# Optimization experiments

Measured on AMD Instinct MI355X. Metric: run time of the kernel, lower is better.

Reference implementation:

```python
import jax, jax.numpy as jnp
import numpy as np


def setup_inputs() -> dict:
    key = jax.random.key(0)
    k_x, k_w1, k_w2 = jax.random.split(key, 3)
    b, d, m, h = 256, 2048, 64, 128  # batch, d_model, history_length, d_out
    lim1 = 1.0 / np.sqrt(m + h)
    lim2 = 1.0 / np.sqrt(h + d)
    x = jax.random.normal(k_x, (b, d, m), dtype=jnp.float32)
    w1 = jax.random.uniform(k_w1, (m, h, d), dtype=jnp.float32, minval=-lim1, maxval=lim1)
    b1 = jnp.zeros((1, h, d), dtype=jnp.float32)
    w2 = jax.random.uniform(k_w2, (h, d), dtype=jnp.float32, minval=-lim2, maxval=lim2)
    b2 = jnp.zeros((1, h), dtype=jnp.float32)
    return {"x": x, "w1": w1, "b1": b1, "w2": w2, "b2": b2}


def reference(x, w1, b1, w2, b2):
    # per-neuron (per-d) MLP: contract over history m, then over hidden h
    hidden = jnp.einsum('bdm,mhd->bhd', x, w1) + b1  # (b, h, d)
    out = jnp.einsum('bhd,hd->bh', hidden, w2) + b2  # (b, h)
    return out
```

## Files before the change

kernel.cpp:

```cpp
#include <hip/hip_runtime.h>

typedef unsigned short u16;
typedef __attribute__((ext_vector_type(8))) short short8;
typedef __attribute__((ext_vector_type(4))) float f32x4;

#define D_TOT 2048
#define M_TOT 64
#define H_TOT 128
#define B_TOT 256
#define NG    256
#define XB    131072
#define W1M   262144

__device__ __forceinline__ u16 f2bf(float f) {
  unsigned u = __builtin_bit_cast(unsigned, f);
  u = (u + 0x7fffu + ((u >> 16) & 1u)) >> 16;
  return (u16)u;
}
__device__ __forceinline__ float bf2f(u16 v) {
  unsigned u = ((unsigned)v) << 16;
  return __builtin_bit_cast(float, u);
}

__global__ __launch_bounds__(256)
void nlm_p0(const float* __restrict__ b1, const float* __restrict__ w2,
            const float* __restrict__ b2, float* __restrict__ ch) {
  const int h = blockIdx.x, t = threadIdx.x;
  const float4* pb = (const float4*)(b1 + (size_t)h * D_TOT);
  const float4* pw = (const float4*)(w2 + (size_t)h * D_TOT);
  float s = 0.f;
  for (int i = t; i < D_TOT / 4; i += 256) {
    float4 a = pb[i], w = pw[i];
    s += a.x * w.x + a.y * w.y + a.z * w.z + a.w * w.w;
  }
  __shared__ float red[256];
  red[t] = s;
  __syncthreads();
  for (int off = 128; off > 0; off >>= 1) {
    if (t < off) red[t] += red[t + off];
    __syncthreads();
  }
  if (t == 0) ch[h] = red[0] + b2[h];
}

__global__ __launch_bounds__(512, 2)
void nlm_main(const float* __restrict__ x, const float* __restrict__ w1,
              const float* __restrict__ w2, u16* __restrict__ partial) {
  __shared__ __align__(16) u16 Bs[8 * H_TOT * 64];
  __shared__ __align__(16) u16 As[2][64 * 72];

  const int tid  = threadIdx.x;
  const int lane = tid & 63, wave = tid >> 6;
  const int g    = ((blockIdx.x & 7) << 5) + (blockIdx.x >> 3);
  const int d0   = g * 8;

  const int a_bl = tid >> 3, a_p = tid & 7;
  const float* xbase = x + (size_t)a_bl * XB + (size_t)d0 * M_TOT + a_p * 8;

  float4 e0 = *(const float4*)(xbase);
  float4 e1 = *(const float4*)(xbase + 4);

  {
    const int m = lane;
#pragma unroll 4
    for (int rep = 0; rep < 16; ++rep) {
      const int h = wave * 16 + rep;
      const float* w1p = w1 + (size_t)m * W1M + (size_t)h * D_TOT + d0;
      const float* w2p = w2 + (size_t)h * D_TOT + d0;
      float4 a0 = *(const float4*)(w1p);
      float4 a1 = *(const float4*)(w1p + 4);
      float4 s0 = *(const float4*)(w2p);
      float4 s1 = *(const float4*)(w2p + 4);
      u16* dst = (u16*)((char*)Bs + h * 128 + ((m * 2) ^ ((h & 7) << 4)));
      dst[0 * 8192] = f2bf(a0.x * s0.x);
      dst[1 * 8192] = f2bf(a0.y * s0.y);
      dst[2 * 8192] = f2bf(a0.z * s0.z);
      dst[3 * 8192] = f2bf(a0.w * s0.w);
      dst[4 * 8192] = f2bf(a1.x * s1.x);
      dst[5 * 8192] = f2bf(a1.y * s1.y);
      dst[6 * 8192] = f2bf(a1.z * s1.z);
      dst[7 * 8192] = f2bf(a1.w * s1.w);
    }
  }
  __syncthreads();

  const int wm = wave >> 2, wn = wave & 3;
  const int quad = lane >> 4, l16 = lane & 15;
  const int q16 = quad * 16;

  int aoff[2][2];
#pragma unroll
  for (int i = 0; i < 2; ++i)
#pragma unroll
    for (int s = 0; s < 2; ++s)
      aoff[i][s] = (wm * 32 + i * 16 + l16) * 72 + s * 32 + quad * 8;

  int boff[2][2];
#pragma unroll
  for (int j = 0; j < 2; ++j) {
    const int hr = wn * 32 + j * 16 + l16;
    const int bx = (hr & 7) << 4;
#pragma unroll
    for (int s = 0; s < 2; ++s)
      boff[j][s] = hr * 128 + ((s * 64 + q16) ^ bx);
  }

  {
    short8 av;
    av[0] = (short)f2bf(e0.x); av[1] = (short)f2bf(e0.y);
    av[2] = (short)f2bf(e0.z); av[3] = (short)f2bf(e0.w);
    av[4] = (short)f2bf(e1.x); av[5] = (short)f2bf(e1.y);
    av[6] = (short)f2bf(e1.z); av[7] = (short)f2bf(e1.w);
    *(short8*)(&As[0][0] + a_bl * 72 + a_p * 8) = av;
  }
  float4 p00, p01, p10, p11;
  {
    const float* xp = xbase + 1 * M_TOT;
    p10 = *(const float4*)(xp);
    p11 = *(const float4*)(xp + 4);
  }
  asm volatile("s_waitcnt lgkmcnt(0)" ::: "memory");
  __builtin_amdgcn_s_barrier();

  f32x4 acc[2][2];

  for (int bq = 0; bq < 4; ++bq) {
#pragma unroll
    for (int i = 0; i < 2; ++i)
#pragma unroll
      for (int j = 0; j < 2; ++j) acc[i][j] = (f32x4){0.f, 0.f, 0.f, 0.f};

#pragma unroll
    for (int c = 0; c < 8; ++c) {
      if (bq < 3 || c < 6) {
        const int bq2 = (c < 6) ? bq : bq + 1;
        const int c2  = (c < 6) ? c + 2 : c - 6;
        const float* xp = xbase + (size_t)bq2 * (64 * (size_t)XB) + c2 * M_TOT;
        if ((c & 1) == 0) { p00 = *(const float4*)(xp); p01 = *(const float4*)(xp + 4); }
        else              { p10 = *(const float4*)(xp); p11 = *(const float4*)(xp + 4); }
      }
      {
        const u16*  Ab = &As[c & 1][0];
        const char* Bb = (const char*)Bs + c * 16384;
#pragma unroll
        for (int s = 0; s < 2; ++s) {
          short8 af0 = *(const short8*)(Ab + aoff[0][s]);
          short8 af1 = *(const short8*)(Ab + aoff[1][s]);
          short8 bf0 = *(const short8*)(Bb + boff[0][s]);
          short8 bf1 = *(const short8*)(Bb + boff[1][s]);
          acc[0][0] = __builtin_amdgcn_mfma_f32_16x16x32_bf16(af0, bf0, acc[0][0], 0, 0, 0);
          acc[0][1] = __builtin_amdgcn_mfma_f32_16x16x32_bf16(af0, bf1, acc[0][1], 0, 0, 0);
          acc[1][0] = __builtin_amdgcn_mfma_f32_16x16x32_bf16(af1, bf0, acc[1][0], 0, 0, 0);
          acc[1][1] = __builtin_amdgcn_mfma_f32_16x16x32_bf16(af1, bf1, acc[1][1], 0, 0, 0);
        }
      }
      if (bq < 3 || c < 7) {
        float4 s0 = ((c + 1) & 1) ? p10 : p00;
        float4 s1 = ((c + 1) & 1) ? p11 : p01;
        short8 av;
        av[0] = (short)f2bf(s0.x); av[1] = (short)f2bf(s0.y);
        av[2] = (short)f2bf(s0.z); av[3] = (short)f2bf(s0.w);
        av[4] = (short)f2bf(s1.x); av[5] = (short)f2bf(s1.y);
        av[6] = (short)f2bf(s1.z); av[7] = (short)f2bf(s1.w);
        *(short8*)(&As[(c + 1) & 1][0] + a_bl * 72 + a_p * 8) = av;
      }
      asm volatile("s_waitcnt lgkmcnt(0)" ::: "memory");
      __builtin_amdgcn_s_barrier();
    }

#pragma unroll
    for (int i = 0; i < 2; ++i)
#pragma unroll
      for (int j = 0; j < 2; ++j) {
        const int hcol = wn * 32 + j * 16 + l16;
#pragma unroll
        for (int r = 0; r < 4; ++r) {
          const int brow = bq * 64 + wm * 32 + i * 16 + quad * 4 + r;
          partial[((size_t)brow * NG + g) * H_TOT + hcol] = f2bf(acc[i][j][r]);
        }
      }
  }
}

__global__ __launch_bounds__(256)
void nlm_p2(const u16* __restrict__ partial, const float* __restrict__ ch,
            float* __restrict__ out) {
  const int b = blockIdx.x, t = threadIdx.x;
  const int h2   = t & 63;
  const int half = t >> 6;
  const u16* base = partial + ((size_t)b * NG + half * 64) * H_TOT + 2 * h2;
  float s0 = 0.f, s1 = 0.f;
#pragma unroll 8
  for (int gg = 0; gg < 64; ++gg) {
    unsigned v = __builtin_nontemporal_load((const unsigned*)(base + (size_t)gg * H_TOT));
    s0 += bf2f((u16)(v & 0xffffu));
    s1 += bf2f((u16)(v >> 16));
  }
  __shared__ float red0[256], red1[256];
  red0[t] = s0;
  red1[t] = s1;
  __syncthreads();
  if (t < 64) {
    float a0 = red0[t] + red0[t + 64] + red0[t + 128] + red0[t + 192];
    float a1 = red1[t] + red1[t + 64] + red1[t + 128] + red1[t + 192];
    out[(size_t)b * H_TOT + 2 * t]     = a0 + ch[2 * t];
    out[(size_t)b * H_TOT + 2 * t + 1] = a1 + ch[2 * t + 1];
  }
}

extern "C" void kernel_launch(void* const* d_in, const int* in_sizes, int n_in,
                              void* d_out, int out_size, void* d_ws, size_t ws_size,
                              hipStream_t stream) {
  const float* x  = (const float*)d_in[0];
  const float* w1 = (const float*)d_in[1];
  const float* b1 = (const float*)d_in[2];
  const float* w2 = (const float*)d_in[3];
  const float* b2 = (const float*)d_in[4];
  float* out = (float*)d_out;

  u16*   partial = (u16*)d_ws;
  float* ch      = (float*)((char*)d_ws + (size_t)B_TOT * NG * H_TOT * sizeof(u16));

  nlm_p0<<<dim3(128),   dim3(256), 0, stream>>>(b1, w2, b2, ch);
  nlm_main<<<dim3(256), dim3(512), 0, stream>>>(x, w1, w2, partial);
  nlm_p2<<<dim3(256),   dim3(256), 0, stream>>>(partial, ch, out);
}
```

Baseline: 266.3 us.

## Load x fragments directly into registers, drop LDS A staging and barriers

The main kernel no longer stages x tiles through a double-buffered LDS array with per-step barriers. Each wave now owns 32 batch rows and all 128 hidden columns, loading its A fragments straight from global memory into registers and issuing 32 MFMAs per k-step. The per-wave tiling changes from 32x32 to 32x128, which raises accumulator register use and drops the software prefetch pipeline. That may expose global load latency and lower occupancy.

```diff
diff --git a/kernel.cpp b/kernel.cpp
--- a/kernel.cpp
+++ b/kernel.cpp
@@ -20,6 +20,14 @@
 __device__ __forceinline__ float bf2f(u16 v) {
   unsigned u = ((unsigned)v) << 16;
   return __builtin_bit_cast(float, u);
+}
+__device__ __forceinline__ short8 pack8(float4 a, float4 b) {
+  short8 t;
+  t[0] = (short)f2bf(a.x); t[1] = (short)f2bf(a.y);
+  t[2] = (short)f2bf(a.z); t[3] = (short)f2bf(a.w);
+  t[4] = (short)f2bf(b.x); t[5] = (short)f2bf(b.y);
+  t[6] = (short)f2bf(b.z); t[7] = (short)f2bf(b.w);
+  return t;
 }
 
 __global__ __launch_bounds__(256)
@@ -47,18 +55,25 @@
 void nlm_main(const float* __restrict__ x, const float* __restrict__ w1,
               const float* __restrict__ w2, u16* __restrict__ partial) {
   __shared__ __align__(16) u16 Bs[8 * H_TOT * 64];
-  __shared__ __align__(16) u16 As[2][64 * 72];
 
   const int tid  = threadIdx.x;
   const int lane = tid & 63, wave = tid >> 6;
   const int g    = ((blockIdx.x & 7) << 5) + (blockIdx.x >> 3);
   const int d0   = g * 8;
-
-  const int a_bl = tid >> 3, a_p = tid & 7;
-  const float* xbase = x + (size_t)a_bl * XB + (size_t)d0 * M_TOT + a_p * 8;
-
-  float4 e0 = *(const float4*)(xbase);
-  float4 e1 = *(const float4*)(xbase + 4);
+  const int quad = lane >> 4, l16 = lane & 15;
+
+  const int wb = wave * 32;
+  const float* xr0 = x + (size_t)(wb + l16) * XB + (size_t)d0 * M_TOT + quad * 8;
+  const float* xr1 = xr0 + (size_t)16 * XB;
+
+  float4 e00a = *(const float4*)(xr0);
+  float4 e00b = *(const float4*)(xr0 + 4);
+  float4 e01a = *(const float4*)(xr0 + 32);
+  float4 e01b = *(const float4*)(xr0 + 36);
+  float4 e10a = *(const float4*)(xr1);
+  float4 e10b = *(const float4*)(xr1 + 4);
+  float4 e11a = *(const float4*)(xr1 + 32);
+  float4 e11b = *(const float4*)(xr1 + 36);
 
   {
     const int m = lane;
@@ -82,104 +97,63 @@
       dst[7 * 8192] = f2bf(a1.w * s1.w);
     }
   }
+
+  int boff[8][2];
+#pragma unroll
+  for (int j = 0; j < 8; ++j) {
+    const int hr = j * 16 + l16;
+    const int bx = (hr & 7) << 4;
+    boff[j][0] = hr * 128 + ((quad * 16) ^ bx);
+    boff[j][1] = hr * 128 + ((64 + quad * 16) ^ bx);
+  }
+
+  f32x4 acc[2][8];
+#pragma unroll
+  for (int i = 0; i < 2; ++i)
+#pragma unroll
+    for (int j = 0; j < 8; ++j) acc[i][j] = (f32x4){0.f, 0.f, 0.f, 0.f};
+
   __syncthreads();
 
-  const int wm = wave >> 2, wn = wave & 3;
-  const int quad = lane >> 4, l16 = lane & 15;
-  const int q16 = quad * 16;
-
-  int aoff[2][2];
+#pragma unroll
+  for (int c = 0; c < 8; ++c) {
+    short8 a00, a01, a10, a11;
+    if (c == 0) {
+      a00 = pack8(e00a, e00b); a01 = pack8(e01a, e01b);
+      a10 = pack8(e10a, e10b); a11 = pack8(e11a, e11b);
+    } else {
+      const float* p0 = xr0 + c * M_TOT;
+      const float* p1 = xr1 + c * M_TOT;
+      a00 = pack8(*(const float4*)(p0),      *(const float4*)(p0 + 4));
+      a01 = pack8(*(const float4*)(p0 + 32), *(const float4*)(p0 + 36));
+      a10 = pack8(*(const float4*)(p1),      *(const float4*)(p1 + 4));
+      a11 = pack8(*(const float4*)(p1 + 32), *(const float4*)(p1 + 36));
+    }
+    const char* Bb = (const char*)Bs + c * 16384;
+#pragma unroll
+    for (int s = 0; s < 2; ++s) {
+      const short8 f0 = s ? a01 : a00;
+      const short8 f1 = s ? a11 : a10;
+#pragma unroll
+      for (int j = 0; j < 8; ++j) {
+        short8 bf = *(const short8*)(Bb + boff[j][s]);
+        acc[0][j] = __builtin_amdgcn_mfma_f32_16x16x32_bf16(f0, bf, acc[0][j], 0, 0, 0);
+        acc[1][j] = __builtin_amdgcn_mfma_f32_16x16x32_bf16(f1, bf, acc[1][j], 0, 0, 0);
+      }
+    }
+  }
+
 #pragma unroll
   for (int i = 0; i < 2; ++i)
 #pragma unroll
-    for (int s = 0; s < 2; ++s)
-      aoff[i][s] = (wm * 32 + i * 16 + l16) * 72 + s * 32 + quad * 8;
-
-  int boff[2][2];
-#pragma unroll
-  for (int j = 0; j < 2; ++j) {
-    const int hr = wn * 32 + j * 16 + l16;
-    const int bx = (hr & 7) << 4;
-#pragma unroll
-    for (int s = 0; s < 2; ++s)
-      boff[j][s] = hr * 128 + ((s * 64 + q16) ^ bx);
-  }
-
-  {
-    short8 av;
-    av[0] = (short)f2bf(e0.x); av[1] = (short)f2bf(e0.y);
-    av[2] = (short)f2bf(e0.z); av[3] = (short)f2bf(e0.w);
-    av[4] = (short)f2bf(e1.x); av[5] = (short)f2bf(e1.y);
-    av[6] = (short)f2bf(e1.z); av[7] = (short)f2bf(e1.w);
-    *(short8*)(&As[0][0] + a_bl * 72 + a_p * 8) = av;
-  }
-  float4 p00, p01, p10, p11;
-  {
-    const float* xp = xbase + 1 * M_TOT;
-    p10 = *(const float4*)(xp);
-    p11 = *(const float4*)(xp + 4);
-  }
-  asm volatile("s_waitcnt lgkmcnt(0)" ::: "memory");
-  __builtin_amdgcn_s_barrier();
-
-  f32x4 acc[2][2];
-
-  for (int bq = 0; bq < 4; ++bq) {
-#pragma unroll
-    for (int i = 0; i < 2; ++i)
-#pragma unroll
-      for (int j = 0; j < 2; ++j) acc[i][j] = (f32x4){0.f, 0.f, 0.f, 0.f};
-
-#pragma unroll
-    for (int c = 0; c < 8; ++c) {
-      if (bq < 3 || c < 6) {
-        const int bq2 = (c < 6) ? bq : bq + 1;
-        const int c2  = (c < 6) ? c + 2 : c - 6;
-        const float* xp = xbase + (size_t)bq2 * (64 * (size_t)XB) + c2 * M_TOT;
-        if ((c & 1) == 0) { p00 = *(const float4*)(xp); p01 = *(const float4*)(xp + 4); }
-        else              { p10 = *(const float4*)(xp); p11 = *(const float4*)(xp + 4); }
+    for (int j = 0; j < 8; ++j) {
+      const int hcol = j * 16 + l16;
+#pragma unroll
+      for (int r = 0; r < 4; ++r) {
+        const int brow = wb + i * 16 + quad * 4 + r;
+        partial[((size_t)brow * NG + g) * H_TOT + hcol] = f2bf(acc[i][j][r]);
       }
-      {
-        const u16*  Ab = &As[c & 1][0];
-        const char* Bb = (const char*)Bs + c * 16384;
-#pragma unroll
-        for (int s = 0; s < 2; ++s) {
-          short8 af0 = *(const short8*)(Ab + aoff[0][s]);
-          short8 af1 = *(const short8*)(Ab + aoff[1][s]);
-          short8 bf0 = *(const short8*)(Bb + boff[0][s]);
-          short8 bf1 = *(const short8*)(Bb + boff[1][s]);
-          acc[0][0] = __builtin_amdgcn_mfma_f32_16x16x32_bf16(af0, bf0, acc[0][0], 0, 0, 0);
-          acc[0][1] = __builtin_amdgcn_mfma_f32_16x16x32_bf16(af0, bf1, acc[0][1], 0, 0, 0);
-          acc[1][0] = __builtin_amdgcn_mfma_f32_16x16x32_bf16(af1, bf0, acc[1][0], 0, 0, 0);
-          acc[1][1] = __builtin_amdgcn_mfma_f32_16x16x32_bf16(af1, bf1, acc[1][1], 0, 0, 0);
-        }
-      }
-      if (bq < 3 || c < 7) {
-        float4 s0 = ((c + 1) & 1) ? p10 : p00;
-        float4 s1 = ((c + 1) & 1) ? p11 : p01;
-        short8 av;
-        av[0] = (short)f2bf(s0.x); av[1] = (short)f2bf(s0.y);
-        av[2] = (short)f2bf(s0.z); av[3] = (short)f2bf(s0.w);
-        av[4] = (short)f2bf(s1.x); av[5] = (short)f2bf(s1.y);
-        av[6] = (short)f2bf(s1.z); av[7] = (short)f2bf(s1.w);
-        *(short8*)(&As[(c + 1) & 1][0] + a_bl * 72 + a_p * 8) = av;
-      }
-      asm volatile("s_waitcnt lgkmcnt(0)" ::: "memory");
-      __builtin_amdgcn_s_barrier();
-    }
-
-#pragma unroll
-    for (int i = 0; i < 2; ++i)
-#pragma unroll
-      for (int j = 0; j < 2; ++j) {
-        const int hcol = wn * 32 + j * 16 + l16;
-#pragma unroll
-        for (int r = 0; r < 4; ++r) {
-          const int brow = bq * 64 + wm * 32 + i * 16 + quad * 4 + r;
-          partial[((size_t)brow * NG + g) * H_TOT + hcol] = f2bf(acc[i][j][r]);
-        }
-      }
-  }
+    }
 }
 
 __global__ __launch_bounds__(256)
```

New measurement: 267.7 us. About the same (+0.5%).
